# Optimization experiments

Measured on AMD Instinct MI355X. Metric: run time of the kernel, lower is better.

Reference implementation:

```python
import jax, jax.numpy as jnp
import numpy as np


def setup_inputs() -> dict:
    key = jax.random.key(0)
    k1, k2 = jax.random.split(key)
    n, t, c, l = 32, 64, 256, 64
    query = jax.random.normal(k1, (n, t, c, l), dtype=jnp.float32)
    key_t = jax.random.normal(k2, (t, n, c), dtype=jnp.float32)
    return {"query": query, "key": key_t}


def reference(query, key):
    # scores[n,l] = sum_{t,c} query[n,t,c,l] * key[t,n,c]
    scores = jnp.einsum('ntcl,tnc->nl', query, key)
    scores = jax.nn.softmax(scores, axis=1)
    # out[t,n,c] = sum_l query[n,t,c,l] * scores[n,l]
    out = jnp.einsum('ntcl,nl->tnc', query, scores)
    return out
```

## Files before the change

### kernel.cpp

```cpp
#include <hip/hip_runtime.h>

#define N 32
#define T 64
#define C 256
#define L 64

__global__ __launch_bounds__(256, 8) void scores_partial_kernel(
    const float* __restrict__ q, const float* __restrict__ k,
    float* __restrict__ partial) {
  const int t    = blockIdx.x;
  const int n    = blockIdx.y;
  const int tid  = threadIdx.x;
  const int lane = tid & 63;
  const int wave = tid >> 6;
  const int sub  = lane >> 4;
  const int lq   = lane & 15;
  const int g    = wave * 4 + sub;

  __shared__ float sk[C];
  __shared__ float sred[4 * L];

  sk[tid] = k[(t * N + n) * C + tid];
  __syncthreads();

  const float* __restrict__ qrow = q + ((size_t)(n * T + t) * C) * L + lq * 4;

  float4 acc = make_float4(0.f, 0.f, 0.f, 0.f);
  #pragma unroll 4
  for (int c = g; c < C; c += 16) {
    const float4 qv = *reinterpret_cast<const float4*>(qrow + (size_t)c * L);
    const float kv = sk[c];
    acc.x = fmaf(qv.x, kv, acc.x);
    acc.y = fmaf(qv.y, kv, acc.y);
    acc.z = fmaf(qv.z, kv, acc.z);
    acc.w = fmaf(qv.w, kv, acc.w);
  }

  acc.x += __shfl_xor(acc.x, 16); acc.y += __shfl_xor(acc.y, 16);
  acc.z += __shfl_xor(acc.z, 16); acc.w += __shfl_xor(acc.w, 16);
  acc.x += __shfl_xor(acc.x, 32); acc.y += __shfl_xor(acc.y, 32);
  acc.z += __shfl_xor(acc.z, 32); acc.w += __shfl_xor(acc.w, 32);

  if (lane < 16) {
    sred[wave * L + lq * 4 + 0] = acc.x;
    sred[wave * L + lq * 4 + 1] = acc.y;
    sred[wave * L + lq * 4 + 2] = acc.z;
    sred[wave * L + lq * 4 + 3] = acc.w;
  }
  __syncthreads();
  if (tid < L) {
    const float s = sred[tid] + sred[L + tid] + sred[2 * L + tid] + sred[3 * L + tid];
    partial[(size_t)t * (N * L) + n * L + tid] = s;
  }
}

__global__ __launch_bounds__(256, 8) void out_kernel(
    const float* __restrict__ q, const float* __restrict__ partial,
    float* __restrict__ out) {
  const int t    = blockIdx.x;
  const int n    = blockIdx.y;
  const int tid  = threadIdx.x;
  const int lane = tid & 63;
  const int wave = tid >> 6;

  __shared__ float sred[4 * L];
  __shared__ __align__(16) float probs[L];

  {
    float s = 0.f;
    #pragma unroll 4
    for (int b = wave * 16; b < wave * 16 + 16; ++b)
      s += partial[(size_t)b * (N * L) + n * L + lane];
    sred[wave * L + lane] = s;
  }
  __syncthreads();
  if (tid < L) {
    float v = sred[tid] + sred[L + tid] + sred[2 * L + tid] + sred[3 * L + tid];
    float m = v;
    #pragma unroll
    for (int off = 32; off > 0; off >>= 1) m = fmaxf(m, __shfl_xor(m, off));
    const float e = __expf(v - m);
    float z = e;
    #pragma unroll
    for (int off = 32; off > 0; off >>= 1) z += __shfl_xor(z, off);
    probs[tid] = e / z;
  }
  __syncthreads();

  const float* __restrict__ qrow = q + ((size_t)((n * T + t) * C + tid)) * L;
  float d = 0.f;
  #pragma unroll 8
  for (int lb = 0; lb < 16; ++lb) {
    const float4 qv = *reinterpret_cast<const float4*>(qrow + lb * 4);
    const float4 pv = *reinterpret_cast<const float4*>(&probs[lb * 4]);
    d += qv.x * pv.x + qv.y * pv.y + qv.z * pv.z + qv.w * pv.w;
  }
  out[(size_t)(t * N + n) * C + tid] = d;
}

extern "C" void kernel_launch(void* const* d_in, const int* in_sizes, int n_in,
                              void* d_out, int out_size, void* d_ws, size_t ws_size,
                              hipStream_t stream) {
  const float* q = (const float*)d_in[0];
  const float* k = (const float*)d_in[1];
  float* out = (float*)d_out;
  float* partial = (float*)d_ws;

  dim3 grid(T, N);
  scores_partial_kernel<<<grid, 256, 0, stream>>>(q, k, partial);
  out_kernel<<<grid, 256, 0, stream>>>(q, partial, out);
}
```

Baseline: 214.0 us.

## Split softmax into its own kernel and coalesce out_kernel query loads with DPP reduction

Moves the cross-t partial-score reduction and softmax out of every out_kernel block into a small separate kernel run once per n, so each out block no longer re-reads all 64 partial rows. out_kernel now reads query with the same coalesced float4 pattern as the scores kernel (16 lanes per c row) and reduces across those lanes with DPP row operations instead of one thread walking a whole row. The scores loop unroll is raised from 4 to 8. The cost is an extra kernel launch and more cross-lane reduction instructions per output element.

```diff
diff --git a/kernel.cpp b/kernel.cpp
--- a/kernel.cpp
+++ b/kernel.cpp
@@ -4,6 +4,19 @@
 #define T 64
 #define C 256
 #define L 64
+
+__device__ __forceinline__ float dpp_allreduce16(float x) {
+  int p;
+  p = __builtin_amdgcn_update_dpp(0, __float_as_int(x), 0x128, 0xf, 0xf, false);
+  x += __int_as_float(p);
+  p = __builtin_amdgcn_update_dpp(0, __float_as_int(x), 0x124, 0xf, 0xf, false);
+  x += __int_as_float(p);
+  p = __builtin_amdgcn_update_dpp(0, __float_as_int(x), 0x4E, 0xf, 0xf, false);
+  x += __int_as_float(p);
+  p = __builtin_amdgcn_update_dpp(0, __float_as_int(x), 0xB1, 0xf, 0xf, false);
+  x += __int_as_float(p);
+  return x;
+}
 
 __global__ __launch_bounds__(256, 8) void scores_partial_kernel(
     const float* __restrict__ q, const float* __restrict__ k,
@@ -26,7 +39,7 @@
   const float* __restrict__ qrow = q + ((size_t)(n * T + t) * C) * L + lq * 4;
 
   float4 acc = make_float4(0.f, 0.f, 0.f, 0.f);
-  #pragma unroll 4
+  #pragma unroll 8
   for (int c = g; c < C; c += 16) {
     const float4 qv = *reinterpret_cast<const float4*>(qrow + (size_t)c * L);
     const float kv = sk[c];
@@ -54,48 +67,47 @@
   }
 }
 
+__global__ __launch_bounds__(64) void softmax_kernel(
+    const float* __restrict__ partial, float* __restrict__ probs) {
+  const int n = blockIdx.x;
+  const int l = threadIdx.x;
+  float s = 0.f;
+  #pragma unroll
+  for (int t = 0; t < T; ++t)
+    s += partial[(size_t)t * (N * L) + n * L + l];
+  float m = s;
+  #pragma unroll
+  for (int off = 32; off > 0; off >>= 1) m = fmaxf(m, __shfl_xor(m, off));
+  const float e = __expf(s - m);
+  float z = e;
+  #pragma unroll
+  for (int off = 32; off > 0; off >>= 1) z += __shfl_xor(z, off);
+  probs[n * L + l] = e / z;
+}
+
 __global__ __launch_bounds__(256, 8) void out_kernel(
-    const float* __restrict__ q, const float* __restrict__ partial,
+    const float* __restrict__ q, const float* __restrict__ probs,
     float* __restrict__ out) {
   const int t    = blockIdx.x;
   const int n    = blockIdx.y;
   const int tid  = threadIdx.x;
   const int lane = tid & 63;
   const int wave = tid >> 6;
+  const int sub  = lane >> 4;
+  const int lq   = lane & 15;
+  const int g    = wave * 4 + sub;
 
-  __shared__ float sred[4 * L];
-  __shared__ __align__(16) float probs[L];
+  const float4 pv = *reinterpret_cast<const float4*>(probs + n * L + lq * 4);
+  const float* __restrict__ qrow = q + ((size_t)(n * T + t) * C) * L + lq * 4;
+  float* __restrict__ orow = out + (size_t)(t * N + n) * C;
 
-  {
-    float s = 0.f;
-    #pragma unroll 4
-    for (int b = wave * 16; b < wave * 16 + 16; ++b)
-      s += partial[(size_t)b * (N * L) + n * L + lane];
-    sred[wave * L + lane] = s;
+  #pragma unroll 8
+  for (int c = g; c < C; c += 16) {
+    const float4 qv = *reinterpret_cast<const float4*>(qrow + (size_t)c * L);
+    float d = qv.x * pv.x + qv.y * pv.y + qv.z * pv.z + qv.w * pv.w;
+    d = dpp_allreduce16(d);
+    if (lq == 0) orow[c] = d;
   }
-  __syncthreads();
-  if (tid < L) {
-    float v = sred[tid] + sred[L + tid] + sred[2 * L + tid] + sred[3 * L + tid];
-    float m = v;
-    #pragma unroll
-    for (int off = 32; off > 0; off >>= 1) m = fmaxf(m, __shfl_xor(m, off));
-    const float e = __expf(v - m);
-    float z = e;
-    #pragma unroll
-    for (int off = 32; off > 0; off >>= 1) z += __shfl_xor(z, off);
-    probs[tid] = e / z;
-  }
-  __syncthreads();
-
-  const float* __restrict__ qrow = q + ((size_t)((n * T + t) * C + tid)) * L;
-  float d = 0.f;
-  #pragma unroll 8
-  for (int lb = 0; lb < 16; ++lb) {
-    const float4 qv = *reinterpret_cast<const float4*>(qrow + lb * 4);
-    const float4 pv = *reinterpret_cast<const float4*>(&probs[lb * 4]);
-    d += qv.x * pv.x + qv.y * pv.y + qv.z * pv.z + qv.w * pv.w;
-  }
-  out[(size_t)(t * N + n) * C + tid] = d;
 }
 
 extern "C" void kernel_launch(void* const* d_in, const int* in_sizes, int n_in,
@@ -105,8 +117,10 @@
   const float* k = (const float*)d_in[1];
   float* out = (float*)d_out;
   float* partial = (float*)d_ws;
+  float* probs   = partial + (size_t)T * N * L;
 
   dim3 grid(T, N);
   scores_partial_kernel<<<grid, 256, 0, stream>>>(q, k, partial);
-  out_kernel<<<grid, 256, 0, stream>>>(q, partial, out);
+  softmax_kernel<<<dim3(N), 64, 0, stream>>>(partial, probs);
+  out_kernel<<<grid, 256, 0, stream>>>(q, probs, out);
 }
```

Result: slower. 227.4 us (+6.3%).

## Fuse score and output kernels with per-batch atomic counter and spin flag

Applied to the files above, without the earlier changes.

Merges the two launches into one kernel. The last tile of each batch to finish, found by an atomic counter, reduces the partials and writes softmax probabilities to global memory, then sets a release flag. All blocks spin on that flag before the output dot product, so each block's query tile is still fresh in cache when it is read again. The grid is 2048 blocks of 256 threads and must all be co-resident (8 per CU), or the spin-wait can deadlock; it also adds a memset and atomic traffic.

```diff
diff --git a/kernel.cpp b/kernel.cpp
--- a/kernel.cpp
+++ b/kernel.cpp
@@ -5,9 +5,12 @@
 #define C 256
 #define L 64
 
-__global__ __launch_bounds__(256, 8) void scores_partial_kernel(
+
+__global__ __launch_bounds__(256, 8) void fused_attn(
     const float* __restrict__ q, const float* __restrict__ k,
-    float* __restrict__ partial) {
+    float* __restrict__ partial, unsigned int* __restrict__ done,
+    unsigned int* __restrict__ flag, float* __restrict__ probs_g,
+    float* __restrict__ out) {
   const int t    = blockIdx.x;
   const int n    = blockIdx.y;
   const int tid  = threadIdx.x;
@@ -19,12 +22,13 @@
 
   __shared__ float sk[C];
   __shared__ float sred[4 * L];
+  __shared__ __align__(16) float probs[L];
+  __shared__ unsigned int s_prev;
 
   sk[tid] = k[(t * N + n) * C + tid];
   __syncthreads();
 
   const float* __restrict__ qrow = q + ((size_t)(n * T + t) * C) * L + lq * 4;
-
   float4 acc = make_float4(0.f, 0.f, 0.f, 0.f);
   #pragma unroll 4
   for (int c = g; c < C; c += 16) {
@@ -35,7 +39,6 @@
     acc.z = fmaf(qv.z, kv, acc.z);
     acc.w = fmaf(qv.w, kv, acc.w);
   }
-
   acc.x += __shfl_xor(acc.x, 16); acc.y += __shfl_xor(acc.y, 16);
   acc.z += __shfl_xor(acc.z, 16); acc.w += __shfl_xor(acc.w, 16);
   acc.x += __shfl_xor(acc.x, 32); acc.y += __shfl_xor(acc.y, 32);
@@ -52,47 +55,56 @@
     const float s = sred[tid] + sred[L + tid] + sred[2 * L + tid] + sred[3 * L + tid];
     partial[(size_t)t * (N * L) + n * L + tid] = s;
   }
-}
 
-__global__ __launch_bounds__(256, 8) void out_kernel(
-    const float* __restrict__ q, const float* __restrict__ partial,
-    float* __restrict__ out) {
-  const int t    = blockIdx.x;
-  const int n    = blockIdx.y;
-  const int tid  = threadIdx.x;
-  const int lane = tid & 63;
-  const int wave = tid >> 6;
+  __threadfence();
+  __syncthreads();
+  if (tid == 0) s_prev = atomicAdd(&done[n], 1u);
+  __syncthreads();
 
-  __shared__ float sred[4 * L];
-  __shared__ __align__(16) float probs[L];
-
-  {
+  if (s_prev == T - 1) {
+    __threadfence();
     float s = 0.f;
     #pragma unroll 4
     for (int b = wave * 16; b < wave * 16 + 16; ++b)
-      s += partial[(size_t)b * (N * L) + n * L + lane];
+      s += __hip_atomic_load(&partial[(size_t)b * (N * L) + n * L + lane],
+                             __ATOMIC_RELAXED, __HIP_MEMORY_SCOPE_AGENT);
     sred[wave * L + lane] = s;
+    __syncthreads();
+    if (tid < L) {
+      float v = sred[tid] + sred[L + tid] + sred[2 * L + tid] + sred[3 * L + tid];
+      float m = v;
+      #pragma unroll
+      for (int off = 32; off > 0; off >>= 1) m = fmaxf(m, __shfl_xor(m, off));
+      const float e = __expf(v - m);
+      float z = e;
+      #pragma unroll
+      for (int off = 32; off > 0; off >>= 1) z += __shfl_xor(z, off);
+      __hip_atomic_store(&probs_g[n * L + tid], e / z,
+                         __ATOMIC_RELAXED, __HIP_MEMORY_SCOPE_AGENT);
+    }
+    __threadfence();
+    __syncthreads();
+    if (tid == 0)
+      __hip_atomic_store(&flag[n], 1u, __ATOMIC_RELEASE, __HIP_MEMORY_SCOPE_AGENT);
+  }
+
+  if (tid == 0) {
+    while (__hip_atomic_load(&flag[n], __ATOMIC_ACQUIRE,
+                             __HIP_MEMORY_SCOPE_AGENT) == 0u)
+      __builtin_amdgcn_s_sleep(8);
   }
   __syncthreads();
-  if (tid < L) {
-    float v = sred[tid] + sred[L + tid] + sred[2 * L + tid] + sred[3 * L + tid];
-    float m = v;
-    #pragma unroll
-    for (int off = 32; off > 0; off >>= 1) m = fmaxf(m, __shfl_xor(m, off));
-    const float e = __expf(v - m);
-    float z = e;
-    #pragma unroll
-    for (int off = 32; off > 0; off >>= 1) z += __shfl_xor(z, off);
-    probs[tid] = e / z;
-  }
+  if (tid < L)
+    probs[tid] = __hip_atomic_load(&probs_g[n * L + tid],
+                                   __ATOMIC_RELAXED, __HIP_MEMORY_SCOPE_AGENT);
   __syncthreads();
 
-  const float* __restrict__ qrow = q + ((size_t)((n * T + t) * C + tid)) * L;
+  const float* __restrict__ q2 = q + ((size_t)((n * T + t) * C + tid)) * L;
   float d = 0.f;
-  #pragma unroll 8
-  for (int lb = 0; lb < 16; ++lb) {
-    const float4 qv = *reinterpret_cast<const float4*>(qrow + lb * 4);
-    const float4 pv = *reinterpret_cast<const float4*>(&probs[lb * 4]);
+  #pragma unroll 4
+  for (int i = 0; i < 16; ++i) {
+    const float4 qv = *reinterpret_cast<const float4*>(q2 + i * 4);
+    const float4 pv = *reinterpret_cast<const float4*>(&probs[i * 4]);
     d += qv.x * pv.x + qv.y * pv.y + qv.z * pv.z + qv.w * pv.w;
   }
   out[(size_t)(t * N + n) * C + tid] = d;
@@ -104,9 +116,15 @@
   const float* q = (const float*)d_in[0];
   const float* k = (const float*)d_in[1];
   float* out = (float*)d_out;
+
   float* partial = (float*)d_ws;
+  unsigned char* base = (unsigned char*)d_ws + (size_t)T * N * L * sizeof(float);
+  unsigned int* done = (unsigned int*)base;
+  unsigned int* flag = done + N;
+  float* probs_g = (float*)(base + 2 * N * sizeof(unsigned int));
+
+  hipMemsetAsync(base, 0, 2 * N * sizeof(unsigned int), stream);
 
   dim3 grid(T, N);
-  scores_partial_kernel<<<grid, 256, 0, stream>>>(q, k, partial);
-  out_kernel<<<grid, 256, 0, stream>>>(q, partial, out);
+  fused_attn<<<grid, 256, 0, stream>>>(q, k, partial, done, flag, probs_g, out);
 }
```

New measurement: 722.9 us. +237.8%, slower.
